# Optimization experiments

Measured on AMD Instinct MI355X. Metric: run time of the kernel, lower is better.

Reference implementation:

```python
import jax, jax.numpy as jnp
import numpy as np

B, S, D = 4, 1024, 2048
H, G = 16, 2            # num_heads, num_groups (GQA)
HD = D // H             # head_dim = 128


def rotate_half(x):
    x1, x2 = x[..., : x.shape[-1] // 2], x[..., x.shape[-1] // 2 :]
    return jnp.concatenate([-x2, x1], axis=-1)


def setup_inputs() -> dict:
    key = jax.random.key(0)
    ks = jax.random.split(key, 9)
    scale = 0.02
    return {
        "x": jax.random.normal(ks[0], (B, S, D), jnp.float32),
        "wq": jax.random.normal(ks[1], (D, D), jnp.float32) * scale,
        "bq": jnp.zeros((D,), jnp.float32),
        "wk": jax.random.normal(ks[2], (D, G * HD), jnp.float32) * scale,
        "bk": jnp.zeros((G * HD,), jnp.float32),
        "wv": jax.random.normal(ks[3], (D, G * HD), jnp.float32) * scale,
        "bv": jnp.zeros((G * HD,), jnp.float32),
        "wo": jax.random.normal(ks[4], (D, D), jnp.float32) * scale,
        "bo": jnp.zeros((D,), jnp.float32),
    }


def reference(x, wq, bq, wk, bk, wv, bv, wo, bo):
    b, s, d = x.shape
    hd = HD
    # projections (flax Linear: y = x @ kernel + bias)
    q = (x @ wq + bq).reshape(b, s, H, hd)
    k = (x @ wk + bk).reshape(b, s, G, hd)
    v = (x @ wv + bv).reshape(b, s, G, hd)

    # RoPE tables (positions = arange(s), matching q_pos/kv_pos defaults)
    inv_freq = 1.0 / 10000 ** (jnp.arange(0, hd, 2, dtype=jnp.float32) / hd)
    t = jnp.arange(s, dtype=jnp.float32)
    freqs = jnp.outer(t, inv_freq)              # [s, hd/2]
    freqs = jnp.concatenate([freqs, freqs], -1)  # [s, hd]
    sin = jnp.sin(freqs)[:, None, :]             # [s, 1, hd]
    cos = jnp.cos(freqs)[:, None, :]

    q = q * cos + rotate_half(q) * sin
    q = q * (hd ** -0.5)  # module's explicit scale
    k = k * cos + rotate_half(k) * sin

    # GQA: expand K/V groups to full heads (repeats = H // G)
    reps = H // G
    k_exp = jnp.repeat(k, reps, axis=2)  # [b, s, H, hd]
    v_exp = jnp.repeat(v, reps, axis=2)

    # jax.nn.dot_product_attention also applies 1/sqrt(hd) by default,
    # so net scaling is hd**-1 (faithful to the original module).
    scores = jnp.einsum("bqhd,bkhd->bhqk", q, k_exp) * (hd ** -0.5)
    attn = jax.nn.softmax(scores, axis=-1)
    out = jnp.einsum("bhqk,bkhd->bqhd", attn, v_exp).reshape(b, s, d)
    return out @ wo + bo
```

## Files before the change

kernel.cpp:

```cpp
#include <hip/hip_runtime.h>
#include <hip/hip_bf16.h>
#include <type_traits>

typedef __attribute__((ext_vector_type(8))) __bf16 bf16x8;
typedef __attribute__((ext_vector_type(4))) float floatx4;

__device__ inline floatx4 mfma_bf16(bf16x8 a, bf16x8 b, floatx4 c) {
    return __builtin_amdgcn_mfma_f32_16x16x32_bf16(a, b, c, 0, 0, 0);
}

__device__ inline void g2l16(const __hip_bfloat16* g, __hip_bfloat16* l) {
    __builtin_amdgcn_global_load_lds(
        (const __attribute__((address_space(1))) void*)g,
        (__attribute__((address_space(3))) void*)l, 16, 0, 0);
}

__device__ inline unsigned pack_bf16x2(float a, float b) {
    __hip_bfloat16 ha = __float2bfloat16(a), hb = __float2bfloat16(b);
    return (unsigned)*(unsigned short*)&ha | ((unsigned)*(unsigned short*)&hb << 16);
}

__global__ void prep_all_k(const float* __restrict__ x,
                           __hip_bfloat16* __restrict__ xb,
                           const float* __restrict__ wq, const float* __restrict__ wk,
                           const float* __restrict__ wv, const float* __restrict__ wo,
                           const float* __restrict__ bq, const float* __restrict__ bk,
                           const float* __restrict__ bv,
                           __hip_bfloat16* __restrict__ wqkvt,
                           __hip_bfloat16* __restrict__ wot,
                           float* __restrict__ bqkv) {
    int bid0 = blockIdx.x;
    if (bid0 < 8192) {
        int i = bid0 * 256 + threadIdx.x;
        float4 v = ((const float4*)x)[i];
        ushort4 u;
        __hip_bfloat16 a0 = __float2bfloat16(v.x), a1 = __float2bfloat16(v.y);
        __hip_bfloat16 a2 = __float2bfloat16(v.z), a3 = __float2bfloat16(v.w);
        u.x = *(unsigned short*)&a0; u.y = *(unsigned short*)&a1;
        u.z = *(unsigned short*)&a2; u.w = *(unsigned short*)&a3;
        ((ushort4*)xb)[i] = u;
        return;
    }
    int bid = bid0 - 8192;
    if (bid >= 9216) {
        int i = (bid - 9216) * 256 + threadIdx.x;
        if (i < 2560)
            bqkv[i] = (i < 2048) ? bq[i] : (i < 2304 ? bk[i - 2048] : bv[i - 2304]);
        return;
    }
    const float* W; __hip_bfloat16* Wt; int C, row_off, cb, rb;
    if (bid < 4096)      { W = wq; Wt = wqkvt; C = 2048; row_off = 0;
                           cb = bid & 63; rb = bid >> 6; }
    else if (bid < 4608) { W = wk; Wt = wqkvt; C = 256;  row_off = 2048;
                           int id = bid - 4096; cb = id & 7; rb = id >> 3; }
    else if (bid < 5120) { W = wv; Wt = wqkvt; C = 256;  row_off = 2304;
                           int id = bid - 4608; cb = id & 7; rb = id >> 3; }
    else                 { W = wo; Wt = wot;   C = 2048; row_off = 0;
                           int id = bid - 5120; cb = id & 63; rb = id >> 6; }
    __shared__ float tile[32][33];
    int c0 = cb * 32, r0 = rb * 32;
    int tx = threadIdx.x & 31, ty0 = threadIdx.x >> 5;
#pragma unroll
    for (int i = 0; i < 4; i++) {
        int ty = ty0 + i * 8;
        tile[ty][tx] = W[(size_t)(r0 + ty) * C + c0 + tx];
    }
    __syncthreads();
#pragma unroll
    for (int i = 0; i < 4; i++) {
        int ty = ty0 + i * 8;
        Wt[(size_t)(row_off + c0 + ty) * 2048 + r0 + tx] = __float2bfloat16(tile[tx][ty]);
    }
}

__global__ __launch_bounds__(256) void gemm_qkv_k(
    const __hip_bfloat16* __restrict__ A,
    const __hip_bfloat16* __restrict__ Bt,
    const float* __restrict__ bias,
    __hip_bfloat16* __restrict__ Qb,
    __hip_bfloat16* __restrict__ Kb,
    __hip_bfloat16* __restrict__ Vlin) {
    __shared__ alignas(16) __hip_bfloat16 As[128 * 32];
    __shared__ alignas(16) __hip_bfloat16 Bs[128 * 32];
    const int t = threadIdx.x, lane = t & 63, w = t >> 6;
    const int quad = lane >> 4, l16 = lane & 15;
    const int bm = blockIdx.y, bn = blockIdx.x;
    const int r_ = t >> 2;
    const int kc_ = (t & 3) ^ ((t >> 3) & 3);
    const int swz = (l16 >> 1) & 3;

    const __hip_bfloat16* gA = A + (size_t)(bm * 128 + r_) * 2048 + kc_ * 8;
    const __hip_bfloat16* gB = Bt + (size_t)(bn * 128 + r_) * 2048 + kc_ * 8;

    floatx4 acc[2][8] = {};

    for (int kt = 0; kt < 2048; kt += 32) {
        g2l16(gA + kt, As + t * 8);
        g2l16(gA + kt + 64 * 2048, As + (t + 256) * 8);
        g2l16(gB + kt, Bs + t * 8);
        g2l16(gB + kt + 64 * 2048, Bs + (t + 256) * 8);
        __syncthreads();
        bf16x8 af[2], bfr[8];
#pragma unroll
        for (int mi = 0; mi < 2; mi++)
            af[mi] = *(const bf16x8*)(As + (w * 32 + mi * 16 + l16) * 32 + (quad ^ swz) * 8);
#pragma unroll
        for (int ni = 0; ni < 8; ni++)
            bfr[ni] = *(const bf16x8*)(Bs + (ni * 16 + l16) * 32 + (quad ^ swz) * 8);
#pragma unroll
        for (int mi = 0; mi < 2; mi++)
#pragma unroll
            for (int ni = 0; ni < 8; ni++)
                acc[mi][ni] = mfma_bf16(af[mi], bfr[ni], acc[mi][ni]);
        __syncthreads();
    }

    const int row_base = bm * 128 + w * 32 + quad * 4;
    if (bn < 18) {
        const float scale = (bn < 16) ? 0.0078125f : 1.0f;
        __hip_bfloat16* dst = (bn < 16) ? Qb : Kb;
        const int nh = (bn < 16) ? 16 : 2;
        const int hh = (bn < 16) ? bn : (bn - 16);
#pragma unroll
        for (int ni = 0; ni < 4; ni++) {
            int j = ni * 16 + l16;
            float invf = __expf(-(float)j * (9.210340371976184f / 64.f));
            float bj  = bias[bn * 128 + j];
            float bj2 = bias[bn * 128 + j + 64];
#pragma unroll
            for (int mi = 0; mi < 2; mi++)
#pragma unroll
                for (int r = 0; r < 4; r++) {
                    int row = row_base + mi * 16 + r;
                    int b = row >> 10, s = row & 1023;
                    float vj  = acc[mi][ni][r] + bj;
                    float vj2 = acc[mi][ni + 4][r] + bj2;
                    float sn, cs;
                    __sincosf((float)s * invf, &sn, &cs);
                    __hip_bfloat16* op = dst + ((size_t)(b * nh + hh) * 1024 + s) * 128;
                    op[j]      = __float2bfloat16((vj * cs - vj2 * sn) * scale);
                    op[j + 64] = __float2bfloat16((vj2 * cs + vj * sn) * scale);
                }
        }
    } else {
        int g = bn - 18;
#pragma unroll
        for (int ni = 0; ni < 8; ni++) {
            int col = ni * 16 + l16;
            float bv = bias[bn * 128 + col];
#pragma unroll
            for (int mi = 0; mi < 2; mi++)
#pragma unroll
                for (int r = 0; r < 4; r++) {
                    int row = row_base + mi * 16 + r;
                    Vlin[(size_t)row * 256 + g * 128 + col] =
                        __float2bfloat16(acc[mi][ni][r] + bv);
                }
        }
    }
}

template <typename OUT_T>
__global__ __launch_bounds__(256) void gemm_bt_k(
    const __hip_bfloat16* __restrict__ A,
    const __hip_bfloat16* __restrict__ Bt,
    const float* __restrict__ bias,
    OUT_T* __restrict__ C,
    int M, int N, int K) {
    __shared__ alignas(16) __hip_bfloat16 As[128 * 32];
    __shared__ alignas(16) __hip_bfloat16 Bs[128 * 32];
    const int t = threadIdx.x;
    const int lane = t & 63;
    const int w = t >> 6;
    const int wm = w & 1, wn = w >> 1;
    const int quad = lane >> 4, l16 = lane & 15;
    const int bm = blockIdx.y, bn = blockIdx.x;
    const int r_ = t >> 2;
    const int kc_ = (t & 3) ^ ((t >> 3) & 3);
    const int swz = (l16 >> 1) & 3;

    const __hip_bfloat16* gA = A + (size_t)(bm * 128 + r_) * K + kc_ * 8;
    const __hip_bfloat16* gB = Bt + (size_t)(bn * 128 + r_) * K + kc_ * 8;

    floatx4 acc[4][4] = {};

    for (int kt = 0; kt < K; kt += 32) {
        g2l16(gA + kt, As + t * 8);
        g2l16(gA + kt + (size_t)64 * K, As + (t + 256) * 8);
        g2l16(gB + kt, Bs + t * 8);
        g2l16(gB + kt + (size_t)64 * K, Bs + (t + 256) * 8);
        __syncthreads();
        bf16x8 af[4], bfr[4];
#pragma unroll
        for (int mi = 0; mi < 4; mi++)
            af[mi] = *(const bf16x8*)(As + (wm * 64 + mi * 16 + l16) * 32 + (quad ^ swz) * 8);
#pragma unroll
        for (int ni = 0; ni < 4; ni++)
            bfr[ni] = *(const bf16x8*)(Bs + (wn * 64 + ni * 16 + l16) * 32 + (quad ^ swz) * 8);
#pragma unroll
        for (int mi = 0; mi < 4; mi++)
#pragma unroll
            for (int ni = 0; ni < 4; ni++)
                acc[mi][ni] = mfma_bf16(af[mi], bfr[ni], acc[mi][ni]);
        __syncthreads();
    }

#pragma unroll
    for (int mi = 0; mi < 4; mi++) {
        int row0 = bm * 128 + wm * 64 + mi * 16 + quad * 4;
#pragma unroll
        for (int ni = 0; ni < 4; ni++) {
            int col = bn * 128 + wn * 64 + ni * 16 + l16;
            float bv = bias[col];
#pragma unroll
            for (int r = 0; r < 4; r++) {
                float v = acc[mi][ni][r] + bv;
                if constexpr (std::is_same<OUT_T, float>::value)
                    C[(size_t)(row0 + r) * N + col] = v;
                else
                    C[(size_t)(row0 + r) * N + col] = __float2bfloat16(v);
            }
        }
    }
}

__global__ void transpose_v_k(const __hip_bfloat16* __restrict__ Vlin,
                              __hip_bfloat16* __restrict__ VT) {
    __shared__ __hip_bfloat16 tile[32][33];
    int bg = blockIdx.z;
    int b = bg >> 1, g = bg & 1;
    int s0 = blockIdx.y * 32, d0 = blockIdx.x * 32;
    int tx = threadIdx.x & 31, ty0 = threadIdx.x >> 5;
#pragma unroll
    for (int i = 0; i < 4; i++) {
        int ty = ty0 + i * 8;
        tile[ty][tx] = Vlin[(size_t)(b * 1024 + s0 + ty) * 256 + g * 128 + d0 + tx];
    }
    __syncthreads();
#pragma unroll
    for (int i = 0; i < 4; i++) {
        int ty = ty0 + i * 8;
        VT[((size_t)(b * 2 + g) * 128 + d0 + ty) * 1024 + s0 + tx] = tile[tx][ty];
    }
}

__global__ __launch_bounds__(256, 3) void attn_k(
    const __hip_bfloat16* __restrict__ Qb,
    const __hip_bfloat16* __restrict__ Kb,
    const __hip_bfloat16* __restrict__ VT,
    __hip_bfloat16* __restrict__ AO) {
    __shared__ alignas(16) __hip_bfloat16 Ks[64 * 128];
    __shared__ alignas(16) __hip_bfloat16 Vs[128 * 64];

    const int bh = blockIdx.x;
    const int b = bh >> 4, h = bh & 15, g = h >> 3;
    const int t = threadIdx.x, lane = t & 63, w = t >> 6;
    const int quad = lane >> 4, l16 = lane & 15;
    const int q0 = blockIdx.y * 64 + w * 16;

    const __hip_bfloat16* Qp = Qb + ((size_t)bh * 1024 + q0 + l16) * 128 + quad * 8;
    bf16x8 aq[4];
#pragma unroll
    for (int kc = 0; kc < 4; kc++)
        aq[kc] = *(const bf16x8*)(Qp + kc * 32);

    const int bg = b * 2 + g;
    const __hip_bfloat16* Kstage = Kb + (size_t)bg * 1024 * 128
        + (t >> 4) * 128 + ((t & 15) ^ (t >> 4)) * 8;
    const __hip_bfloat16* Vstage = VT + (size_t)bg * 128 * 1024
        + (t >> 3) * 1024 + ((t & 7) ^ ((t >> 3) & 7)) * 8;

    const int qs0lane = l16 + ((quad & 1) << 5);
    const int qs1lane = qs0lane + 16;
    const int hi = quad >> 1;

    float l_part = 0.f;
    floatx4 o[8] = {};

    for (int kv = 0; kv < 1024; kv += 64) {
#pragma unroll
        for (int j = 0; j < 4; j++)
            g2l16(Kstage + (size_t)(kv + j * 16) * 128, Ks + (j * 256 + t) * 8);
#pragma unroll
        for (int j = 0; j < 4; j++)
            g2l16(Vstage + (size_t)j * 32 * 1024 + kv, Vs + (j * 256 + t) * 8);
        __syncthreads();

        floatx4 s[4] = {};
#pragma unroll
        for (int nj = 0; nj < 4; nj++)
#pragma unroll
            for (int kc = 0; kc < 4; kc++) {
                bf16x8 kb = *(const bf16x8*)(Ks + (nj * 16 + l16) * 128
                                             + (((kc * 4 + quad) ^ l16) * 8));
                s[nj] = mfma_bf16(kb, aq[kc], s[nj]);
            }

        unsigned pk[4][2];
#pragma unroll
        for (int nj = 0; nj < 4; nj++) {
            float p0 = __expf(s[nj][0]), p1 = __expf(s[nj][1]);
            float p2 = __expf(s[nj][2]), p3 = __expf(s[nj][3]);
            l_part += (p0 + p1) + (p2 + p3);
            pk[nj][0] = pack_bf16x2(p0, p1);
            pk[nj][1] = pack_bf16x2(p2, p3);
        }

        bf16x8 ap[2];
#pragma unroll
        for (int kc2 = 0; kc2 < 2; kc2++) {
            unsigned v00 = __shfl(pk[2 * kc2][0],     qs0lane);
            unsigned v01 = __shfl(pk[2 * kc2][1],     qs0lane);
            unsigned v02 = __shfl(pk[2 * kc2][0],     qs1lane);
            unsigned v03 = __shfl(pk[2 * kc2][1],     qs1lane);
            unsigned v10 = __shfl(pk[2 * kc2 + 1][0], qs0lane);
            unsigned v11 = __shfl(pk[2 * kc2 + 1][1], qs0lane);
            unsigned v12 = __shfl(pk[2 * kc2 + 1][0], qs1lane);
            unsigned v13 = __shfl(pk[2 * kc2 + 1][1], qs1lane);
            unsigned u0 = hi ? v10 : v00;
            unsigned u1 = hi ? v11 : v01;
            unsigned u2 = hi ? v12 : v02;
            unsigned u3 = hi ? v13 : v03;
            unsigned arr[4] = {u0, u1, u2, u3};
            ap[kc2] = *(const bf16x8*)arr;
        }

#pragma unroll
        for (int ni = 0; ni < 8; ni++)
#pragma unroll
            for (int kc2 = 0; kc2 < 2; kc2++) {
                bf16x8 vb = *(const bf16x8*)(Vs + (ni * 16 + l16) * 64
                                             + (((kc2 * 4 + quad) ^ (l16 & 7)) * 8));
                o[ni] = mfma_bf16(ap[kc2], vb, o[ni]);
            }
        __syncthreads();
    }

    l_part += __shfl_xor(l_part, 16);
    l_part += __shfl_xor(l_part, 32);
    float invl = 1.f / l_part;
    float invr[4];
#pragma unroll
    for (int r = 0; r < 4; r++)
        invr[r] = __shfl(invl, quad * 4 + r);

#pragma unroll
    for (int r = 0; r < 4; r++) {
        size_t srow = (size_t)b * 1024 + q0 + quad * 4 + r;
#pragma unroll
        for (int ni = 0; ni < 8; ni++)
            AO[srow * 2048 + h * 128 + ni * 16 + l16] =
                __float2bfloat16(o[ni][r] * invr[r]);
    }
}

extern "C" void kernel_launch(void* const* d_in, const int* in_sizes, int n_in,
                              void* d_out, int out_size, void* d_ws, size_t ws_size,
                              hipStream_t stream) {
    (void)in_sizes; (void)n_in; (void)out_size; (void)ws_size;
    const float* x  = (const float*)d_in[0];
    const float* wq = (const float*)d_in[1];
    const float* bq = (const float*)d_in[2];
    const float* wk = (const float*)d_in[3];
    const float* bk = (const float*)d_in[4];
    const float* wv = (const float*)d_in[5];
    const float* bv = (const float*)d_in[6];
    const float* wo = (const float*)d_in[7];
    const float* bo = (const float*)d_in[8];
    float* out = (float*)d_out;

    char* ws = (char*)d_ws;
    __hip_bfloat16* xb    = (__hip_bfloat16*)(ws + 0);
    __hip_bfloat16* AO    = xb;
    __hip_bfloat16* wqkvt = (__hip_bfloat16*)(ws + 16777216);
    __hip_bfloat16* wot   = (__hip_bfloat16*)(ws + 27262976);
    __hip_bfloat16* Qb    = (__hip_bfloat16*)(ws + 35651584);
    __hip_bfloat16* Kb    = (__hip_bfloat16*)(ws + 52428800);
    __hip_bfloat16* Vlin  = (__hip_bfloat16*)(ws + 54525952);
    __hip_bfloat16* VT    = (__hip_bfloat16*)(ws + 56623104);
    float*          bqkv  = (float*)(ws + 58720256);

    prep_all_k<<<17418, 256, 0, stream>>>(x, xb, wq, wk, wv, wo, bq, bk, bv,
                                          wqkvt, wot, bqkv);
    gemm_qkv_k<<<dim3(20, 32), 256, 0, stream>>>(xb, wqkvt, bqkv, Qb, Kb, Vlin);
    transpose_v_k<<<dim3(4, 32, 8), 256, 0, stream>>>(Vlin, VT);
    attn_k<<<dim3(64, 16), 256, 0, stream>>>(Qb, Kb, VT, AO);
    gemm_bt_k<float><<<dim3(16, 32), 256, 0, stream>>>(AO, wot, bo, out, 4096, 2048, 2048);
}
```

Before: 283.4 us.

## Fuse V transpose into QKV GEMM epilogue and double query rows per attention wave

The QKV GEMM epilogue now transposes the V tile through shared memory and writes VT directly, so the separate transpose kernel and the Vlin round trip go away. The attention kernel gives each wave 32 query rows instead of 16, which reuses every K/V fragment loaded from LDS across two MFMA streams and halves the grid. Softmax switches to exp2f, with log2(e) folded into the Q scale. The change raises register pressure, so launch bounds drop from 3 to 2 blocks per CU, and the grid now has 512 blocks.

```diff
diff --git a/kernel.cpp b/kernel.cpp
--- a/kernel.cpp
+++ b/kernel.cpp
@@ -79,7 +79,7 @@
     const float* __restrict__ bias,
     __hip_bfloat16* __restrict__ Qb,
     __hip_bfloat16* __restrict__ Kb,
-    __hip_bfloat16* __restrict__ Vlin) {
+    __hip_bfloat16* __restrict__ VT) {
     __shared__ alignas(16) __hip_bfloat16 As[128 * 32];
     __shared__ alignas(16) __hip_bfloat16 Bs[128 * 32];
     const int t = threadIdx.x, lane = t & 63, w = t >> 6;
@@ -117,7 +117,7 @@
 
     const int row_base = bm * 128 + w * 32 + quad * 4;
     if (bn < 18) {
-        const float scale = (bn < 16) ? 0.0078125f : 1.0f;
+        const float scale = (bn < 16) ? 0.011271367439545085f : 1.0f;
         __hip_bfloat16* dst = (bn < 16) ? Qb : Kb;
         const int nh = (bn < 16) ? 16 : 2;
         const int hh = (bn < 16) ? bn : (bn - 16);
@@ -143,19 +143,30 @@
                 }
         }
     } else {
-        int g = bn - 18;
-#pragma unroll
-        for (int ni = 0; ni < 8; ni++) {
-            int col = ni * 16 + l16;
-            float bv = bias[bn * 128 + col];
-#pragma unroll
-            for (int mi = 0; mi < 2; mi++)
-#pragma unroll
-                for (int r = 0; r < 4; r++) {
-                    int row = row_base + mi * 16 + r;
-                    Vlin[(size_t)row * 256 + g * 128 + col] =
-                        __float2bfloat16(acc[mi][ni][r] + bv);
-                }
+        const int g = bn - 18;
+        __hip_bfloat16 (*vt)[128] = (__hip_bfloat16 (*)[128])As;
+        const int b2 = bm >> 3, s0 = (bm & 7) * 128;
+        const size_t vbase = ((size_t)((b2 * 2 + g) * 128)) * 1024 + s0;
+        const int d_ = t >> 3, s8 = (t & 7) * 16;
+#pragma unroll
+        for (int p = 0; p < 4; p++) {
+            __syncthreads();
+#pragma unroll
+            for (int nn = 0; nn < 2; nn++) {
+                int ni = 2 * p + nn;
+                float bv = bias[bn * 128 + ni * 16 + l16];
+#pragma unroll
+                for (int mi = 0; mi < 2; mi++)
+#pragma unroll
+                    for (int r = 0; r < 4; r++)
+                        vt[nn * 16 + l16][w * 32 + mi * 16 + quad * 4 + r] =
+                            __float2bfloat16(acc[mi][ni][r] + bv);
+            }
+            __syncthreads();
+            bf16x8 v0 = *(const bf16x8*)&vt[d_][s8];
+            bf16x8 v1 = *(const bf16x8*)&vt[d_][s8 + 8];
+            *(bf16x8*)(VT + vbase + (size_t)(p * 32 + d_) * 1024 + s8) = v0;
+            *(bf16x8*)(VT + vbase + (size_t)(p * 32 + d_) * 1024 + s8 + 8) = v1;
         }
     }
 }
@@ -224,27 +235,7 @@
     }
 }
 
-__global__ void transpose_v_k(const __hip_bfloat16* __restrict__ Vlin,
-                              __hip_bfloat16* __restrict__ VT) {
-    __shared__ __hip_bfloat16 tile[32][33];
-    int bg = blockIdx.z;
-    int b = bg >> 1, g = bg & 1;
-    int s0 = blockIdx.y * 32, d0 = blockIdx.x * 32;
-    int tx = threadIdx.x & 31, ty0 = threadIdx.x >> 5;
-#pragma unroll
-    for (int i = 0; i < 4; i++) {
-        int ty = ty0 + i * 8;
-        tile[ty][tx] = Vlin[(size_t)(b * 1024 + s0 + ty) * 256 + g * 128 + d0 + tx];
-    }
-    __syncthreads();
-#pragma unroll
-    for (int i = 0; i < 4; i++) {
-        int ty = ty0 + i * 8;
-        VT[((size_t)(b * 2 + g) * 128 + d0 + ty) * 1024 + s0 + tx] = tile[tx][ty];
-    }
-}
-
-__global__ __launch_bounds__(256, 3) void attn_k(
+__global__ __launch_bounds__(256, 2) void attn_k(
     const __hip_bfloat16* __restrict__ Qb,
     const __hip_bfloat16* __restrict__ Kb,
     const __hip_bfloat16* __restrict__ VT,
@@ -256,13 +247,15 @@
     const int b = bh >> 4, h = bh & 15, g = h >> 3;
     const int t = threadIdx.x, lane = t & 63, w = t >> 6;
     const int quad = lane >> 4, l16 = lane & 15;
-    const int q0 = blockIdx.y * 64 + w * 16;
+    const int q0 = blockIdx.y * 128 + w * 32;
 
     const __hip_bfloat16* Qp = Qb + ((size_t)bh * 1024 + q0 + l16) * 128 + quad * 8;
-    bf16x8 aq[4];
-#pragma unroll
-    for (int kc = 0; kc < 4; kc++)
-        aq[kc] = *(const bf16x8*)(Qp + kc * 32);
+    bf16x8 aq[2][4];
+#pragma unroll
+    for (int mi = 0; mi < 2; mi++)
+#pragma unroll
+        for (int kc = 0; kc < 4; kc++)
+            aq[mi][kc] = *(const bf16x8*)(Qp + mi * 16 * 128 + kc * 32);
 
     const int bg = b * 2 + g;
     const __hip_bfloat16* Kstage = Kb + (size_t)bg * 1024 * 128
@@ -274,8 +267,8 @@
     const int qs1lane = qs0lane + 16;
     const int hi = quad >> 1;
 
-    float l_part = 0.f;
-    floatx4 o[8] = {};
+    float l_part[2] = {};
+    floatx4 o[2][8] = {};
 
     for (int kv = 0; kv < 1024; kv += 64) {
 #pragma unroll
@@ -286,44 +279,49 @@
             g2l16(Vstage + (size_t)j * 32 * 1024 + kv, Vs + (j * 256 + t) * 8);
         __syncthreads();
 
-        floatx4 s[4] = {};
+        floatx4 s[2][4] = {};
 #pragma unroll
         for (int nj = 0; nj < 4; nj++)
 #pragma unroll
             for (int kc = 0; kc < 4; kc++) {
                 bf16x8 kb = *(const bf16x8*)(Ks + (nj * 16 + l16) * 128
                                              + (((kc * 4 + quad) ^ l16) * 8));
-                s[nj] = mfma_bf16(kb, aq[kc], s[nj]);
-            }
-
-        unsigned pk[4][2];
-#pragma unroll
-        for (int nj = 0; nj < 4; nj++) {
-            float p0 = __expf(s[nj][0]), p1 = __expf(s[nj][1]);
-            float p2 = __expf(s[nj][2]), p3 = __expf(s[nj][3]);
-            l_part += (p0 + p1) + (p2 + p3);
-            pk[nj][0] = pack_bf16x2(p0, p1);
-            pk[nj][1] = pack_bf16x2(p2, p3);
-        }
-
-        bf16x8 ap[2];
-#pragma unroll
-        for (int kc2 = 0; kc2 < 2; kc2++) {
-            unsigned v00 = __shfl(pk[2 * kc2][0],     qs0lane);
-            unsigned v01 = __shfl(pk[2 * kc2][1],     qs0lane);
-            unsigned v02 = __shfl(pk[2 * kc2][0],     qs1lane);
-            unsigned v03 = __shfl(pk[2 * kc2][1],     qs1lane);
-            unsigned v10 = __shfl(pk[2 * kc2 + 1][0], qs0lane);
-            unsigned v11 = __shfl(pk[2 * kc2 + 1][1], qs0lane);
-            unsigned v12 = __shfl(pk[2 * kc2 + 1][0], qs1lane);
-            unsigned v13 = __shfl(pk[2 * kc2 + 1][1], qs1lane);
-            unsigned u0 = hi ? v10 : v00;
-            unsigned u1 = hi ? v11 : v01;
-            unsigned u2 = hi ? v12 : v02;
-            unsigned u3 = hi ? v13 : v03;
-            unsigned arr[4] = {u0, u1, u2, u3};
-            ap[kc2] = *(const bf16x8*)arr;
-        }
+                s[0][nj] = mfma_bf16(kb, aq[0][kc], s[0][nj]);
+                s[1][nj] = mfma_bf16(kb, aq[1][kc], s[1][nj]);
+            }
+
+        unsigned pk[2][4][2];
+#pragma unroll
+        for (int mi = 0; mi < 2; mi++)
+#pragma unroll
+            for (int nj = 0; nj < 4; nj++) {
+                float p0 = exp2f(s[mi][nj][0]), p1 = exp2f(s[mi][nj][1]);
+                float p2 = exp2f(s[mi][nj][2]), p3 = exp2f(s[mi][nj][3]);
+                l_part[mi] += (p0 + p1) + (p2 + p3);
+                pk[mi][nj][0] = pack_bf16x2(p0, p1);
+                pk[mi][nj][1] = pack_bf16x2(p2, p3);
+            }
+
+        bf16x8 ap[2][2];
+#pragma unroll
+        for (int mi = 0; mi < 2; mi++)
+#pragma unroll
+            for (int kc2 = 0; kc2 < 2; kc2++) {
+                unsigned v00 = __shfl(pk[mi][2 * kc2][0],     qs0lane);
+                unsigned v01 = __shfl(pk[mi][2 * kc2][1],     qs0lane);
+                unsigned v02 = __shfl(pk[mi][2 * kc2][0],     qs1lane);
+                unsigned v03 = __shfl(pk[mi][2 * kc2][1],     qs1lane);
+                unsigned v10 = __shfl(pk[mi][2 * kc2 + 1][0], qs0lane);
+                unsigned v11 = __shfl(pk[mi][2 * kc2 + 1][1], qs0lane);
+                unsigned v12 = __shfl(pk[mi][2 * kc2 + 1][0], qs1lane);
+                unsigned v13 = __shfl(pk[mi][2 * kc2 + 1][1], qs1lane);
+                unsigned u0 = hi ? v10 : v00;
+                unsigned u1 = hi ? v11 : v01;
+                unsigned u2 = hi ? v12 : v02;
+                unsigned u3 = hi ? v13 : v03;
+                unsigned arr[4] = {u0, u1, u2, u3};
+                ap[mi][kc2] = *(const bf16x8*)arr;
+            }
 
 #pragma unroll
         for (int ni = 0; ni < 8; ni++)
@@ -331,26 +329,30 @@
             for (int kc2 = 0; kc2 < 2; kc2++) {
                 bf16x8 vb = *(const bf16x8*)(Vs + (ni * 16 + l16) * 64
                                              + (((kc2 * 4 + quad) ^ (l16 & 7)) * 8));
-                o[ni] = mfma_bf16(ap[kc2], vb, o[ni]);
-            }
-        __syncthreads();
-    }
-
-    l_part += __shfl_xor(l_part, 16);
-    l_part += __shfl_xor(l_part, 32);
-    float invl = 1.f / l_part;
-    float invr[4];
-#pragma unroll
-    for (int r = 0; r < 4; r++)
-        invr[r] = __shfl(invl, quad * 4 + r);
-
-#pragma unroll
-    for (int r = 0; r < 4; r++) {
-        size_t srow = (size_t)b * 1024 + q0 + quad * 4 + r;
-#pragma unroll
-        for (int ni = 0; ni < 8; ni++)
-            AO[srow * 2048 + h * 128 + ni * 16 + l16] =
-                __float2bfloat16(o[ni][r] * invr[r]);
+                o[0][ni] = mfma_bf16(ap[0][kc2], vb, o[0][ni]);
+                o[1][ni] = mfma_bf16(ap[1][kc2], vb, o[1][ni]);
+            }
+        __syncthreads();
+    }
+
+#pragma unroll
+    for (int mi = 0; mi < 2; mi++) {
+        float lp = l_part[mi];
+        lp += __shfl_xor(lp, 16);
+        lp += __shfl_xor(lp, 32);
+        float invl = 1.f / lp;
+        float invr[4];
+#pragma unroll
+        for (int r = 0; r < 4; r++)
+            invr[r] = __shfl(invl, quad * 4 + r);
+#pragma unroll
+        for (int r = 0; r < 4; r++) {
+            size_t srow = (size_t)b * 1024 + q0 + mi * 16 + quad * 4 + r;
+#pragma unroll
+            for (int ni = 0; ni < 8; ni++)
+                AO[srow * 2048 + h * 128 + ni * 16 + l16] =
+                    __float2bfloat16(o[mi][ni][r] * invr[r]);
+        }
     }
 }
 
@@ -376,14 +378,12 @@
     __hip_bfloat16* wot   = (__hip_bfloat16*)(ws + 27262976);
     __hip_bfloat16* Qb    = (__hip_bfloat16*)(ws + 35651584);
     __hip_bfloat16* Kb    = (__hip_bfloat16*)(ws + 52428800);
-    __hip_bfloat16* Vlin  = (__hip_bfloat16*)(ws + 54525952);
     __hip_bfloat16* VT    = (__hip_bfloat16*)(ws + 56623104);
     float*          bqkv  = (float*)(ws + 58720256);
 
     prep_all_k<<<17418, 256, 0, stream>>>(x, xb, wq, wk, wv, wo, bq, bk, bv,
                                           wqkvt, wot, bqkv);
-    gemm_qkv_k<<<dim3(20, 32), 256, 0, stream>>>(xb, wqkvt, bqkv, Qb, Kb, Vlin);
-    transpose_v_k<<<dim3(4, 32, 8), 256, 0, stream>>>(Vlin, VT);
-    attn_k<<<dim3(64, 16), 256, 0, stream>>>(Qb, Kb, VT, AO);
+    gemm_qkv_k<<<dim3(20, 32), 256, 0, stream>>>(xb, wqkvt, bqkv, Qb, Kb, VT);
+    attn_k<<<dim3(64, 8), 256, 0, stream>>>(Qb, Kb, VT, AO);
     gemm_bt_k<float><<<dim3(16, 32), 256, 0, stream>>>(AO, wot, bo, out, 4096, 2048, 2048);
 }
```

Result: no change. 282.9 us (-0.2%).
